# Performance work log

Measured on AMD Instinct MI355X. Metric: run time of the kernel, lower is better.

Reference implementation:

```python
import jax, jax.numpy as jnp
import numpy as np

GAMMA = 1.0   # soft-min temperature of the differentiable DP
BIG = 1e9     # stand-in for +inf (keeps vjp NaN-free; underflows to 0 weight in softmin)


def setup_inputs() -> dict:
    key = jax.random.key(0)
    # batched pairwise cost matrix for the alignment DP
    input_array = jax.random.uniform(key, (512, 256, 256), dtype=jnp.float32)
    return {"input_array": input_array}


def reference(input_array):
    """Soft-min alignment DP (edit-distance/soft-DTW style), antidiagonal wavefront.

    D[i,j] = C[i,j] + softmin_gamma(D[i-1,j], D[i,j-1], D[i-1,j-1]); returns D[S-1,S-1].
    Diagonal k holds cells (i, j=k-i); carry = last two diagonals.
    """
    B, S, _ = input_array.shape
    i = jnp.arange(S)
    k = jnp.arange(2 * S - 1)
    js = k[:, None] - i[None, :]                 # [2S-1, S] column index j = k - i
    valid = (js >= 0) & (js < S)                 # which lanes of each diagonal exist
    js_c = jnp.clip(js, 0, S - 1)

    # pack cost diagonals: cd[k, b, i] = C[b, i, k-i]   -> [2S-1, B, S]
    cd = input_array[:, i[None, :], js_c]        # [B, 2S-1, S]
    cd = jnp.transpose(cd, (1, 0, 2))

    d0 = jnp.where(i == 0, cd[0], BIG)           # diagonal k=0: only cell (0,0)
    dm1 = jnp.full((B, S), BIG, input_array.dtype)

    def softmin(stk):                            # stk: [3, B, S]
        return -GAMMA * jax.nn.logsumexp(-stk / GAMMA, axis=0)

    def shift(d):                                # index i -> i-1, pad with BIG
        return jnp.concatenate([jnp.full((B, 1), BIG, d.dtype), d[:, :-1]], axis=1)

    def step(carry, xs):
        d1, d2 = carry                           # diagonals k-1, k-2
        c_k, v_k = xs
        # predecessors of (i, k-i): (i,j-1)->d1[i], (i-1,j)->d1[i-1], (i-1,j-1)->d2[i-1]
        preds = jnp.stack([d1, shift(d1), shift(d2)])
        d = c_k + softmin(preds)
        d = jnp.where(v_k[None, :], d, BIG)
        return (d, d1), None

    (d_last, _), _ = jax.lax.scan(step, (d0, dm1), (cd[1:], valid[1:]))
    return d_last[:, S - 1]                      # D[S-1, S-1] per batch -> [B]
```

## Files before the change

### kernel.cpp

```cpp
#include <hip/hip_runtime.h>

#define S 256
#define L2E 1.44269504088896340736f
#define LN2 0.69314718055994530942f

#define EXP2F(x) __builtin_amdgcn_exp2f(x)
#define LOG2F(x) __builtin_amdgcn_logf(x)


template <int I> __device__ __forceinline__ float comp(const float4& v) {
    if constexpr (I == 0) return v.x;
    else if constexpr (I == 1) return v.y;
    else if constexpr (I == 2) return v.z;
    else return v.w;
}

__device__ __forceinline__ float4 g4f(const float4& v) {
    float4 r;
    r.x = EXP2F(v.x * -L2E); r.y = EXP2F(v.y * -L2E);
    r.z = EXP2F(v.z * -L2E); r.w = EXP2F(v.w * -L2E);
    return r;
}

template <int P, int SB>
__device__ __forceinline__ void stepf(
    int kk, int t, int t4, const float* __restrict__ Cb,
    int rb0, int rb1, int rb2, int rb3,
    float4& c0, float4& c1, float4& c2, float4& c3,
    float4& n0, float4& n1, float4& n2, float4& n3,
    float4& s00, float4& s01, float4& s02, float4& s03,
    float4& s10, float4& s11, float4& s12, float4& s13,
    float4& s20, float4& s21, float4& s22, float4& s23,
    float4& s30, float4& s31, float4& s32, float4& s33,
    float& w10, float& w11, float& w12, float& w13,
    float& w20, float& w21, float& w22, float& w23,
    float& pd1, float& pd2)
{
    const int colr = kk + (20 - P) - t4;
    const int col  = colr < 0 ? 0 : (colr > 252 ? 252 : colr);
    const int rb   = (P == 0) ? rb0 : (P == 1) ? rb1 : (P == 2) ? rb2 : rb3;
    const float4 ld = *(const float4*)(Cb + rb + col);

    float4& cP = (P == 0) ? c0 : (P == 1) ? c1 : (P == 2) ? c2 : c3;
    float4& nP = (P == 0) ? n0 : (P == 1) ? n1 : (P == 2) ? n2 : n3;
    float4& sP =
        (SB == 0) ? ((P == 0) ? s00 : (P == 1) ? s01 : (P == 2) ? s02 : s03)
      : (SB == 1) ? ((P == 0) ? s10 : (P == 1) ? s11 : (P == 2) ? s12 : s13)
      : (SB == 2) ? ((P == 0) ? s20 : (P == 1) ? s21 : (P == 2) ? s22 : s23)
                  : ((P == 0) ? s30 : (P == 1) ? s31 : (P == 2) ? s32 : s33);

    const bool junk = (colr > 268);
    float4 gq;
    gq.x = junk ? 0.0f : EXP2F(sP.x * -L2E);
    gq.y = junk ? 0.0f : EXP2F(sP.y * -L2E);
    gq.z = junk ? 0.0f : EXP2F(sP.z * -L2E);
    gq.w = junk ? 0.0f : EXP2F(sP.w * -L2E);
    cP = nP;
    nP = gq;
    sP = ld;

    const float g0 = comp<(P    ) & 3>(c0);
    const float g1 = comp<(P + 3) & 3>(c1);
    const float g2 = comp<(P + 2) & 3>(c2);
    const float g3 = comp<(P + 1) & 3>(c3);

    const float e0 = g0 * (w10 + pd1 + pd2);
    const float e1 = g1 * (w11 + w10 + w20);
    const float e2 = g2 * (w12 + w11 + w21);
    const float e3 = g3 * (w13 + w12 + w22);

    w20 = w10; w21 = w11; w22 = w12; w23 = w13;
    w10 = e0;  w11 = e1;  w12 = e2;  w13 = e3;

    const float nx = __shfl_up(e3, 1);
    pd2 = pd1;
    pd1 = (t == 0) ? 0.0f : nx;
}

__global__ __launch_bounds__(64, 1) void dp_softmin_wave(const float* __restrict__ C,
                                                         float* __restrict__ out) {
    const int b = blockIdx.x;
    const int t = threadIdx.x;
    const float* Cb = C + ((size_t)b << 16);
    const int t4 = 4 * t;

    const int rb0 = (t4 + 0) << 8;
    const int rb1 = (t4 + 1) << 8;
    const int rb2 = (t4 + 2) << 8;
    const int rb3 = (t4 + 3) << 8;

    auto cl = [](int c) { return c < 0 ? 0 : (c > 252 ? 252 : c); };
    auto q  = [&](int rb, int col) { return *(const float4*)(Cb + rb + col); };

    float4 c0 = g4f(q(rb0, 0)), c1 = g4f(q(rb1, 0)),
           c2 = g4f(q(rb2, 0)), c3 = g4f(q(rb3, 0));
    float4 n0 = g4f(q(rb0, cl(4 - t4)));
    float4 n1 = c1, n2 = c2, n3 = c3;

    float4 s00 = q(rb0, cl(20 - t4));
    float4 s01 = q(rb1, cl(4 - t4));
    float4 s02 = q(rb2, cl(4 - t4));
    float4 s03 = q(rb3, cl(4 - t4));
    float4 s10 = q(rb0, cl(8 - t4)),  s11 = q(rb1, cl(8 - t4));
    float4 s12 = q(rb2, cl(8 - t4)),  s13 = q(rb3, cl(8 - t4));
    float4 s20 = q(rb0, cl(12 - t4)), s21 = q(rb1, cl(12 - t4));
    float4 s22 = q(rb2, cl(12 - t4)), s23 = q(rb3, cl(12 - t4));
    float4 s30 = q(rb0, cl(16 - t4)), s31 = q(rb1, cl(16 - t4));
    float4 s32 = q(rb2, cl(16 - t4)), s33 = q(rb3, cl(16 - t4));

    float w10 = 0.0f, w11 = 0.0f, w12 = 0.0f, w13 = 0.0f;
    float w20 = 0.0f, w21 = 0.0f, w22 = 0.0f, w23 = 0.0f;
    float pd1 = 0.0f, pd2 = 0.0f;
    int sig = 0;

    if (t == 0) w10 = c0.x;

#define ARGS t, t4, Cb, rb0, rb1, rb2, rb3, c0,c1,c2,c3, n0,n1,n2,n3, \
             s00,s01,s02,s03, s10,s11,s12,s13, s20,s21,s22,s23, s30,s31,s32,s33, \
             w10,w11,w12,w13, w20,w21,w22,w23, pd1,pd2

    stepf<1,0>(1, ARGS);  stepf<2,0>(2, ARGS);  stepf<3,0>(3, ARGS);
    stepf<0,1>(4, ARGS);  stepf<1,1>(5, ARGS);  stepf<2,1>(6, ARGS);  stepf<3,1>(7, ARGS);
    stepf<0,2>(8, ARGS);  stepf<1,2>(9, ARGS);  stepf<2,2>(10, ARGS); stepf<3,2>(11, ARGS);
    stepf<0,3>(12, ARGS); stepf<1,3>(13, ARGS); stepf<2,3>(14, ARGS); stepf<3,3>(15, ARGS);

#pragma clang loop unroll(disable)
    for (int kb = 16; kb <= 480; kb += 16) {
        if ((kb & 63) == 0) {
            float M = fmaxf(fmaxf(fmaxf(w10, w11), fmaxf(w12, w13)),
                            fmaxf(fmaxf(w20, w21), fmaxf(w22, w23)));
            #pragma unroll
            for (int m = 1; m < 64; m <<= 1) M = fmaxf(M, __shfl_xor(M, m));
            int e = ((__float_as_int(M) >> 23) & 255) - 127;
            float f = __int_as_float((127 - e) << 23);
            w10 *= f; w11 *= f; w12 *= f; w13 *= f;
            w20 *= f; w21 *= f; w22 *= f; w23 *= f;
            pd1 *= f; pd2 *= f;
            sig -= e;
        }
        stepf<0,0>(kb + 0, ARGS);  stepf<1,0>(kb + 1, ARGS);
        stepf<2,0>(kb + 2, ARGS);  stepf<3,0>(kb + 3, ARGS);
        stepf<0,1>(kb + 4, ARGS);  stepf<1,1>(kb + 5, ARGS);
        stepf<2,1>(kb + 6, ARGS);  stepf<3,1>(kb + 7, ARGS);
        stepf<0,2>(kb + 8, ARGS);  stepf<1,2>(kb + 9, ARGS);
        stepf<2,2>(kb + 10, ARGS); stepf<3,2>(kb + 11, ARGS);
        stepf<0,3>(kb + 12, ARGS); stepf<1,3>(kb + 13, ARGS);
        stepf<2,3>(kb + 14, ARGS); stepf<3,3>(kb + 15, ARGS);
    }

    stepf<0,0>(496, ARGS); stepf<1,0>(497, ARGS); stepf<2,0>(498, ARGS); stepf<3,0>(499, ARGS);
    stepf<0,1>(500, ARGS); stepf<1,1>(501, ARGS); stepf<2,1>(502, ARGS); stepf<3,1>(503, ARGS);
    stepf<0,2>(504, ARGS); stepf<1,2>(505, ARGS); stepf<2,2>(506, ARGS); stepf<3,2>(507, ARGS);
    stepf<0,3>(508, ARGS); stepf<1,3>(509, ARGS); stepf<2,3>(510, ARGS);
#undef ARGS

    if (t == 63) out[b] = ((float)sig - LOG2F(w13)) * LN2;
}

extern "C" void kernel_launch(void* const* d_in, const int* in_sizes, int n_in,
                              void* d_out, int out_size, void* d_ws, size_t ws_size,
                              hipStream_t stream) {
    const float* C = (const float*)d_in[0];
    float* out = (float*)d_out;
    dp_softmin_wave<<<512, 64, 0, stream>>>(C, out);
}
```

Measured before the change: 68.50 us.

## Stage cost matrix through swizzled LDS with coalesced global loads and ping-pong state

Replaces per-step strided global float4 loads of cost-matrix rows with coalesced global loads of tiles that are staged into a swizzled 64KB LDS buffer. The DP steps then read LDS two steps ahead. The diagonal state is also kept in alternating register sets (wa/wb) to avoid per-step register copies. Relying on single-wave ordering instead of explicit barriers for LDS visibility adds complexity and correctness risk, and LDS latency now sits in the dependency chain.

Result: slower. 90.42 us (+32.0%).

```diff
diff --git a/kernel.cpp b/kernel.cpp
--- a/kernel.cpp
+++ b/kernel.cpp
@@ -1,6 +1,5 @@
 #include <hip/hip_runtime.h>
 
-#define S 256
 #define L2E 1.44269504088896340736f
 #define LN2 0.69314718055994530942f
 
@@ -22,59 +21,81 @@
     return r;
 }
 
-template <int P, int SB>
-__device__ __forceinline__ void stepf(
-    int kk, int t, int t4, const float* __restrict__ Cb,
-    int rb0, int rb1, int rb2, int rb3,
-    float4& c0, float4& c1, float4& c2, float4& c3,
-    float4& n0, float4& n1, float4& n2, float4& n3,
-    float4& s00, float4& s01, float4& s02, float4& s03,
-    float4& s10, float4& s11, float4& s12, float4& s13,
-    float4& s20, float4& s21, float4& s22, float4& s23,
-    float4& s30, float4& s31, float4& s32, float4& s33,
-    float& w10, float& w11, float& w12, float& w13,
-    float& w20, float& w21, float& w22, float& w23,
+template <int P>
+__device__ __forceinline__ float4 lds_rd(const float4* lds4, int kkq,
+    int rr0,int rr1,int rr2,int rr3, int AA0,int AA1,int AA2,int AA3,
+    int qq0,int qq1,int qq2,int qq3)
+{
+    const int rr = (P==0)?rr0:(P==1)?rr1:(P==2)?rr2:rr3;
+    const int AA = (P==0)?AA0:(P==1)?AA1:(P==2)?AA2:AA3;
+    const int qq = (P==0)?qq0:(P==1)?qq1:(P==2)?qq2:qq3;
+    int u = kkq + 4 - rr;
+    int ucl = u < 0 ? 0 : (u > 252 ? 252 : u);
+    int cidx = AA + (((ucl >> 4) & 3) << 10) + ((((ucl >> 2) & 3) ^ qq));
+    return lds4[cidx];
+}
+
+template <int G>
+__device__ __forceinline__ void stage_load(int sigma, const float* __restrict__ Cb,
+    int v0,int v1,int v2,int v3, float4& L)
+{
+    int w = sigma - G;
+    if (0 <= w && w < 16) {
+        constexpr int p = G & 3;
+        const int vo = (p==0)?v0:(p==1)?v1:(p==2)?v2:v3;
+        L = *(const float4*)(Cb + 4096*G + 16*w + vo);
+    }
+}
+
+template <int G>
+__device__ __forceinline__ void stage_write(int sigma, float4* lds4, int t, const float4& L)
+{
+    int w = sigma - G;
+    if (0 <= w && w < 16)
+        lds4[((w & 3) * 16 + G) * 64 + t] = L;
+}
+
+template <int P>
+__device__ __forceinline__ void stepf(int kk, int t, float4* lds4,
+    int rr0,int rr1,int rr2,int rr3, int AA0,int AA1,int AA2,int AA3,
+    int qq0,int qq1,int qq2,int qq3,
+    float4& RQ,
+    float4& c0,float4& c1,float4& c2,float4& c3,
+    float4& n0,float4& n1,float4& n2,float4& n3,
+    float& w10,float& w11,float& w12,float& w13,
+    float& w20,float& w21,float& w22,float& w23,
     float& pd1, float& pd2)
 {
-    const int colr = kk + (20 - P) - t4;
-    const int col  = colr < 0 ? 0 : (colr > 252 ? 252 : colr);
-    const int rb   = (P == 0) ? rb0 : (P == 1) ? rb1 : (P == 2) ? rb2 : rb3;
-    const float4 ld = *(const float4*)(Cb + rb + col);
-
-    float4& cP = (P == 0) ? c0 : (P == 1) ? c1 : (P == 2) ? c2 : c3;
-    float4& nP = (P == 0) ? n0 : (P == 1) ? n1 : (P == 2) ? n2 : n3;
-    float4& sP =
-        (SB == 0) ? ((P == 0) ? s00 : (P == 1) ? s01 : (P == 2) ? s02 : s03)
-      : (SB == 1) ? ((P == 0) ? s10 : (P == 1) ? s11 : (P == 2) ? s12 : s13)
-      : (SB == 2) ? ((P == 0) ? s20 : (P == 1) ? s21 : (P == 2) ? s22 : s23)
-                  : ((P == 0) ? s30 : (P == 1) ? s31 : (P == 2) ? s32 : s33);
-
-    const bool junk = (colr > 268);
+    const int rr = (P==0)?rr0:(P==1)?rr1:(P==2)?rr2:rr3;
+    int u = kk + 4 - rr;
+    int ucl = u < 0 ? 0 : (u > 252 ? 252 : u);
+    bool ok = (u == ucl);
     float4 gq;
-    gq.x = junk ? 0.0f : EXP2F(sP.x * -L2E);
-    gq.y = junk ? 0.0f : EXP2F(sP.y * -L2E);
-    gq.z = junk ? 0.0f : EXP2F(sP.z * -L2E);
-    gq.w = junk ? 0.0f : EXP2F(sP.w * -L2E);
+    gq.x = ok ? EXP2F(RQ.x * -L2E) : 0.0f;
+    gq.y = ok ? EXP2F(RQ.y * -L2E) : 0.0f;
+    gq.z = ok ? EXP2F(RQ.z * -L2E) : 0.0f;
+    gq.w = ok ? EXP2F(RQ.w * -L2E) : 0.0f;
+    float4& cP = (P==0)?c0:(P==1)?c1:(P==2)?c2:c3;
+    float4& nP = (P==0)?n0:(P==1)?n1:(P==2)?n2:n3;
     cP = nP;
     nP = gq;
-    sP = ld;
 
     const float g0 = comp<(P    ) & 3>(c0);
     const float g1 = comp<(P + 3) & 3>(c1);
     const float g2 = comp<(P + 2) & 3>(c2);
     const float g3 = comp<(P + 1) & 3>(c3);
-
     const float e0 = g0 * (w10 + pd1 + pd2);
     const float e1 = g1 * (w11 + w10 + w20);
     const float e2 = g2 * (w12 + w11 + w21);
     const float e3 = g3 * (w13 + w12 + w22);
-
-    w20 = w10; w21 = w11; w22 = w12; w23 = w13;
-    w10 = e0;  w11 = e1;  w12 = e2;  w13 = e3;
+    w20 = e0; w21 = e1; w22 = e2; w23 = e3;
 
     const float nx = __shfl_up(e3, 1);
     pd2 = pd1;
     pd1 = (t == 0) ? 0.0f : nx;
+
+    RQ = lds_rd<(P + 2) & 3>(lds4, kk + 2, rr0,rr1,rr2,rr3,
+                             AA0,AA1,AA2,AA3, qq0,qq1,qq2,qq3);
 }
 
 __global__ __launch_bounds__(64, 1) void dp_softmin_wave(const float* __restrict__ C,
@@ -84,77 +105,156 @@
     const float* Cb = C + ((size_t)b << 16);
     const int t4 = 4 * t;
 
-    const int rb0 = (t4 + 0) << 8;
-    const int rb1 = (t4 + 1) << 8;
-    const int rb2 = (t4 + 2) << 8;
-    const int rb3 = (t4 + 3) << 8;
+    __shared__ float4 lds4[4096];
+
+    int rr0, rr1, rr2, rr3, AA0, AA1, AA2, AA3, qq0, qq1, qq2, qq3;
+    {
+        int r, g, q, qp;
+        r = t4 + 0; g = r >> 4; q = r & 15; qp = q ^ (q >> 3);
+        rr0 = r; AA0 = g * 64 + qp * 4; qq0 = ((q >> 1) & 3) ^ (g & 3);
+        r = t4 + 1; g = r >> 4; q = r & 15; qp = q ^ (q >> 3);
+        rr1 = r; AA1 = g * 64 + qp * 4; qq1 = ((q >> 1) & 3) ^ (g & 3);
+        r = t4 + 2; g = r >> 4; q = r & 15; qp = q ^ (q >> 3);
+        rr2 = r; AA2 = g * 64 + qp * 4; qq2 = ((q >> 1) & 3) ^ (g & 3);
+        r = t4 + 3; g = r >> 4; q = r & 15; qp = q ^ (q >> 3);
+        rr3 = r; AA3 = g * 64 + qp * 4; qq3 = ((q >> 1) & 3) ^ (g & 3);
+    }
+    const int qW  = (t >> 2) ^ (t >> 5);
+    const int mmb = (t & 3) ^ ((qW >> 1) & 3);
+    const int voff0 = 256 * qW + 4 * (mmb ^ 0);
+    const int voff1 = 256 * qW + 4 * (mmb ^ 1);
+    const int voff2 = 256 * qW + 4 * (mmb ^ 2);
+    const int voff3 = 256 * qW + 4 * (mmb ^ 3);
 
     auto cl = [](int c) { return c < 0 ? 0 : (c > 252 ? 252 : c); };
-    auto q  = [&](int rb, int col) { return *(const float4*)(Cb + rb + col); };
-
-    float4 c0 = g4f(q(rb0, 0)), c1 = g4f(q(rb1, 0)),
-           c2 = g4f(q(rb2, 0)), c3 = g4f(q(rb3, 0));
-    float4 n0 = g4f(q(rb0, cl(4 - t4)));
+    auto q4 = [&](int rb, int col) { return *(const float4*)(Cb + rb + col); };
+    const int rb0 = (t4 + 0) << 8, rb1 = (t4 + 1) << 8,
+              rb2 = (t4 + 2) << 8, rb3 = (t4 + 3) << 8;
+    float4 c0 = g4f(q4(rb0, 0)), c1 = g4f(q4(rb1, 0)),
+           c2 = g4f(q4(rb2, 0)), c3 = g4f(q4(rb3, 0));
+    float4 n0 = g4f(q4(rb0, cl(4 - t4)));
     float4 n1 = c1, n2 = c2, n3 = c3;
 
-    float4 s00 = q(rb0, cl(20 - t4));
-    float4 s01 = q(rb1, cl(4 - t4));
-    float4 s02 = q(rb2, cl(4 - t4));
-    float4 s03 = q(rb3, cl(4 - t4));
-    float4 s10 = q(rb0, cl(8 - t4)),  s11 = q(rb1, cl(8 - t4));
-    float4 s12 = q(rb2, cl(8 - t4)),  s13 = q(rb3, cl(8 - t4));
-    float4 s20 = q(rb0, cl(12 - t4)), s21 = q(rb1, cl(12 - t4));
-    float4 s22 = q(rb2, cl(12 - t4)), s23 = q(rb3, cl(12 - t4));
-    float4 s30 = q(rb0, cl(16 - t4)), s31 = q(rb1, cl(16 - t4));
-    float4 s32 = q(rb2, cl(16 - t4)), s33 = q(rb3, cl(16 - t4));
-
-    float w10 = 0.0f, w11 = 0.0f, w12 = 0.0f, w13 = 0.0f;
-    float w20 = 0.0f, w21 = 0.0f, w22 = 0.0f, w23 = 0.0f;
+    float wa0 = 0.0f, wa1 = 0.0f, wa2 = 0.0f, wa3 = 0.0f;
+    float wb0 = 0.0f, wb1 = 0.0f, wb2 = 0.0f, wb3 = 0.0f;
     float pd1 = 0.0f, pd2 = 0.0f;
     int sig = 0;
-
-    if (t == 0) w10 = c0.x;
-
-#define ARGS t, t4, Cb, rb0, rb1, rb2, rb3, c0,c1,c2,c3, n0,n1,n2,n3, \
-             s00,s01,s02,s03, s10,s11,s12,s13, s20,s21,s22,s23, s30,s31,s32,s33, \
-             w10,w11,w12,w13, w20,w21,w22,w23, pd1,pd2
-
-    stepf<1,0>(1, ARGS);  stepf<2,0>(2, ARGS);  stepf<3,0>(3, ARGS);
-    stepf<0,1>(4, ARGS);  stepf<1,1>(5, ARGS);  stepf<2,1>(6, ARGS);  stepf<3,1>(7, ARGS);
-    stepf<0,2>(8, ARGS);  stepf<1,2>(9, ARGS);  stepf<2,2>(10, ARGS); stepf<3,2>(11, ARGS);
-    stepf<0,3>(12, ARGS); stepf<1,3>(13, ARGS); stepf<2,3>(14, ARGS); stepf<3,3>(15, ARGS);
+    if (t == 0) wa0 = c0.x;
+
+    float4 P00 = *(const float4*)(Cb + 0    + voff0);
+    float4 P10 = *(const float4*)(Cb + 4096 + voff1);
+    float4 P01 = *(const float4*)(Cb + 16   + voff0);
+    lds4[   0 + t] = P00;
+    lds4[  64 + t] = P10;
+    lds4[1024 + t] = P01;
+    float4 RQ0, RQ1;
+    RQ1 = lds_rd<1>(lds4, 1, rr0,rr1,rr2,rr3, AA0,AA1,AA2,AA3, qq0,qq1,qq2,qq3);
+    RQ0 = lds_rd<2>(lds4, 2, rr0,rr1,rr2,rr3, AA0,AA1,AA2,AA3, qq0,qq1,qq2,qq3);
+
+#define VOFFS voff0, voff1, voff2, voff3
+#define CONSTS rr0,rr1,rr2,rr3, AA0,AA1,AA2,AA3, qq0,qq1,qq2,qq3
+#define STEP_AB(kk, P, RQx) stepf<P>(kk, t, lds4, CONSTS, RQx, c0,c1,c2,c3, n0,n1,n2,n3, \
+        wa0,wa1,wa2,wa3, wb0,wb1,wb2,wb3, pd1, pd2)
+#define STEP_BA(kk, P, RQx) stepf<P>(kk, t, lds4, CONSTS, RQx, c0,c1,c2,c3, n0,n1,n2,n3, \
+        wb0,wb1,wb2,wb3, wa0,wa1,wa2,wa3, pd1, pd2)
+
+    {
+        float4 L0, L1, L2, L3, L4, L5, L6, L7, L8, L9, L10, L11, L12, L13, L14, L15;
+        stage_load<0>(2, Cb, VOFFS, L0);
+        stage_load<1>(2, Cb, VOFFS, L1);
+        stage_load<2>(2, Cb, VOFFS, L2);  stage_load<3>(2, Cb, VOFFS, L3);
+        STEP_AB(1, 1, RQ1);
+        stage_load<4>(2, Cb, VOFFS, L4);  stage_load<5>(2, Cb, VOFFS, L5);
+        STEP_BA(2, 2, RQ0);
+        stage_load<6>(2, Cb, VOFFS, L6);  stage_load<7>(2, Cb, VOFFS, L7);
+        STEP_AB(3, 3, RQ1);
+        stage_load<8>(2, Cb, VOFFS, L8);  stage_load<9>(2, Cb, VOFFS, L9);
+        stage_write<0>(2, lds4, t, L0);   stage_write<1>(2, lds4, t, L1);
+        STEP_BA(4, 0, RQ0);
+        stage_load<10>(2, Cb, VOFFS, L10); stage_load<11>(2, Cb, VOFFS, L11);
+        stage_write<2>(2, lds4, t, L2);   stage_write<3>(2, lds4, t, L3);
+        STEP_AB(5, 1, RQ1);
+        stage_load<12>(2, Cb, VOFFS, L12); stage_load<13>(2, Cb, VOFFS, L13);
+        stage_write<4>(2, lds4, t, L4);   stage_write<5>(2, lds4, t, L5);
+        STEP_BA(6, 2, RQ0);
+        stage_load<14>(2, Cb, VOFFS, L14); stage_load<15>(2, Cb, VOFFS, L15);
+        stage_write<6>(2, lds4, t, L6);   stage_write<7>(2, lds4, t, L7);
+        STEP_AB(7, 3, RQ1);
+        stage_write<8>(2, lds4, t, L8);   stage_write<9>(2, lds4, t, L9);
+        STEP_BA(8, 0, RQ0);
+        stage_write<10>(2, lds4, t, L10); stage_write<11>(2, lds4, t, L11);
+        STEP_AB(9, 1, RQ1);
+        stage_write<12>(2, lds4, t, L12); stage_write<13>(2, lds4, t, L13);
+        STEP_BA(10, 2, RQ0);
+        stage_write<14>(2, lds4, t, L14); stage_write<15>(2, lds4, t, L15);
+        STEP_AB(11, 3, RQ1);
+        STEP_BA(12, 0, RQ0);
+        STEP_AB(13, 1, RQ1);
+        STEP_BA(14, 2, RQ0);
+        STEP_AB(15, 3, RQ1);
+    }
 
 #pragma clang loop unroll(disable)
     for (int kb = 16; kb <= 480; kb += 16) {
         if ((kb & 63) == 0) {
-            float M = fmaxf(fmaxf(fmaxf(w10, w11), fmaxf(w12, w13)),
-                            fmaxf(fmaxf(w20, w21), fmaxf(w22, w23)));
+            float M = fmaxf(fmaxf(fmaxf(wa0, wa1), fmaxf(wa2, wa3)),
+                            fmaxf(fmaxf(wb0, wb1), fmaxf(wb2, wb3)));
             #pragma unroll
             for (int m = 1; m < 64; m <<= 1) M = fmaxf(M, __shfl_xor(M, m));
             int e = ((__float_as_int(M) >> 23) & 255) - 127;
             float f = __int_as_float((127 - e) << 23);
-            w10 *= f; w11 *= f; w12 *= f; w13 *= f;
-            w20 *= f; w21 *= f; w22 *= f; w23 *= f;
+            wa0 *= f; wa1 *= f; wa2 *= f; wa3 *= f;
+            wb0 *= f; wb1 *= f; wb2 *= f; wb3 *= f;
             pd1 *= f; pd2 *= f;
             sig -= e;
         }
-        stepf<0,0>(kb + 0, ARGS);  stepf<1,0>(kb + 1, ARGS);
-        stepf<2,0>(kb + 2, ARGS);  stepf<3,0>(kb + 3, ARGS);
-        stepf<0,1>(kb + 4, ARGS);  stepf<1,1>(kb + 5, ARGS);
-        stepf<2,1>(kb + 6, ARGS);  stepf<3,1>(kb + 7, ARGS);
-        stepf<0,2>(kb + 8, ARGS);  stepf<1,2>(kb + 9, ARGS);
-        stepf<2,2>(kb + 10, ARGS); stepf<3,2>(kb + 11, ARGS);
-        stepf<0,3>(kb + 12, ARGS); stepf<1,3>(kb + 13, ARGS);
-        stepf<2,3>(kb + 14, ARGS); stepf<3,3>(kb + 15, ARGS);
-    }
-
-    stepf<0,0>(496, ARGS); stepf<1,0>(497, ARGS); stepf<2,0>(498, ARGS); stepf<3,0>(499, ARGS);
-    stepf<0,1>(500, ARGS); stepf<1,1>(501, ARGS); stepf<2,1>(502, ARGS); stepf<3,1>(503, ARGS);
-    stepf<0,2>(504, ARGS); stepf<1,2>(505, ARGS); stepf<2,2>(506, ARGS); stepf<3,2>(507, ARGS);
-    stepf<0,3>(508, ARGS); stepf<1,3>(509, ARGS); stepf<2,3>(510, ARGS);
-#undef ARGS
-
-    if (t == 63) out[b] = ((float)sig - LOG2F(w13)) * LN2;
+        const int sigma = (kb >> 4) + 2;
+        float4 L0, L1, L2, L3, L4, L5, L6, L7, L8, L9, L10, L11, L12, L13, L14, L15;
+        stage_load<0>(sigma, Cb, VOFFS, L0);  stage_load<1>(sigma, Cb, VOFFS, L1);
+        STEP_BA(kb + 0, 0, RQ0);
+        stage_load<2>(sigma, Cb, VOFFS, L2);  stage_load<3>(sigma, Cb, VOFFS, L3);
+        STEP_AB(kb + 1, 1, RQ1);
+        stage_load<4>(sigma, Cb, VOFFS, L4);  stage_load<5>(sigma, Cb, VOFFS, L5);
+        STEP_BA(kb + 2, 2, RQ0);
+        stage_load<6>(sigma, Cb, VOFFS, L6);  stage_load<7>(sigma, Cb, VOFFS, L7);
+        STEP_AB(kb + 3, 3, RQ1);
+        stage_load<8>(sigma, Cb, VOFFS, L8);  stage_load<9>(sigma, Cb, VOFFS, L9);
+        stage_write<0>(sigma, lds4, t, L0);   stage_write<1>(sigma, lds4, t, L1);
+        STEP_BA(kb + 4, 0, RQ0);
+        stage_load<10>(sigma, Cb, VOFFS, L10); stage_load<11>(sigma, Cb, VOFFS, L11);
+        stage_write<2>(sigma, lds4, t, L2);   stage_write<3>(sigma, lds4, t, L3);
+        STEP_AB(kb + 5, 1, RQ1);
+        stage_load<12>(sigma, Cb, VOFFS, L12); stage_load<13>(sigma, Cb, VOFFS, L13);
+        stage_write<4>(sigma, lds4, t, L4);   stage_write<5>(sigma, lds4, t, L5);
+        STEP_BA(kb + 6, 2, RQ0);
+        stage_load<14>(sigma, Cb, VOFFS, L14); stage_load<15>(sigma, Cb, VOFFS, L15);
+        stage_write<6>(sigma, lds4, t, L6);   stage_write<7>(sigma, lds4, t, L7);
+        STEP_AB(kb + 7, 3, RQ1);
+        stage_write<8>(sigma, lds4, t, L8);   stage_write<9>(sigma, lds4, t, L9);
+        STEP_BA(kb + 8, 0, RQ0);
+        stage_write<10>(sigma, lds4, t, L10); stage_write<11>(sigma, lds4, t, L11);
+        STEP_AB(kb + 9, 1, RQ1);
+        stage_write<12>(sigma, lds4, t, L12); stage_write<13>(sigma, lds4, t, L13);
+        STEP_BA(kb + 10, 2, RQ0);
+        stage_write<14>(sigma, lds4, t, L14); stage_write<15>(sigma, lds4, t, L15);
+        STEP_AB(kb + 11, 3, RQ1);
+        STEP_BA(kb + 12, 0, RQ0);
+        STEP_AB(kb + 13, 1, RQ1);
+        STEP_BA(kb + 14, 2, RQ0);
+        STEP_AB(kb + 15, 3, RQ1);
+    }
+
+    STEP_BA(496, 0, RQ0); STEP_AB(497, 1, RQ1); STEP_BA(498, 2, RQ0); STEP_AB(499, 3, RQ1);
+    STEP_BA(500, 0, RQ0); STEP_AB(501, 1, RQ1); STEP_BA(502, 2, RQ0); STEP_AB(503, 3, RQ1);
+    STEP_BA(504, 0, RQ0); STEP_AB(505, 1, RQ1); STEP_BA(506, 2, RQ0); STEP_AB(507, 3, RQ1);
+    STEP_BA(508, 0, RQ0); STEP_AB(509, 1, RQ1); STEP_BA(510, 2, RQ0);
+
+#undef STEP_AB
+#undef STEP_BA
+#undef VOFFS
+#undef CONSTS
+
+    if (t == 63) out[b] = ((float)sig - LOG2F(wa3)) * LN2;
 }
 
 extern "C" void kernel_launch(void* const* d_in, const int* in_sizes, int n_in,
```
